# Kernel tuning notes

Hardware: AMD Instinct MI355X
Metric: run time of the kernel (lower is better)

The kernel has to match this reference:

```python
import jax, jax.numpy as jnp
import numpy as np

N, M, DIM, HEADS = 32768, 2048, 128, 8
TAU = 0.1


def setup_inputs() -> dict:
    key = jax.random.key(0)
    ks = jax.random.split(key, 7)
    return {
        "x1": jax.random.normal(ks[0], (N, DIM), jnp.float32),
        "k": jax.random.normal(ks[1], (N, DIM), jnp.float32),
        "c": jax.random.normal(ks[2], (M, DIM), jnp.float32),
        "Wq": jax.random.normal(ks[3], (DIM * HEADS, DIM), jnp.float32) * 0.02,
        "bq": jax.random.normal(ks[4], (DIM * HEADS,), jnp.float32) * 0.02,
        "Wd": jax.random.normal(ks[5], (DIM, DIM), jnp.float32) * 0.02,
        "bd": jax.random.normal(ks[6], (DIM,), jnp.float32) * 0.02,
    }


def reference(x1, k, c, Wq, bq, Wd, bd):
    # q and k both go through the same 'query' projection (as in the source)
    q = x1 @ Wq.T + bq                      # [N, dim*H]
    kq = k @ Wq.T + bq                      # [N, dim*H]
    C = jnp.tile(c, (1, HEADS))             # torch.cat([c]*H, dim=1) -> [M, dim*H]
    t = q + kq                              # additive attention 'scores' input
    logits = (t @ C.T) / jnp.sqrt(jnp.asarray(DIM, t.dtype))  # [N, M]
    p = jax.nn.softmax(logits, axis=-1)
    # gumbel_softmax(p, tau=0.1, hard=True): -log(Exp(1)) ~ Gumbel(0,1)
    noise = jax.random.gumbel(jax.random.key(42), p.shape, p.dtype)
    y_soft = jax.nn.softmax((p + noise) / TAU, axis=-1)
    idx = jnp.argmax(y_soft, axis=-1)
    y_hard = jax.nn.one_hot(idx, M, dtype=p.dtype)
    y = y_hard - jax.lax.stop_gradient(y_soft) + y_soft  # straight-through
    # attention_dropout and dropout are rate 0.0 -> identity
    out = y.T @ x1                          # [M, dim]
    return out @ Wd.T + bd                  # dense
```

## Files before the change

kernel.cpp:

```cpp
#include <hip/hip_runtime.h>
#include <stdint.h>
#include <math.h>

#define NROW 32768
#define MCOL 2048
#define KDIM 128
#define NHEAD 8
#define SCALE 0.08838834764831845f

typedef __attribute__((ext_vector_type(8))) short short8;
typedef __attribute__((ext_vector_type(4))) float f32x4;

__device__ __forceinline__ uint32_t rotl32(uint32_t x, uint32_t r) {
  return __builtin_amdgcn_alignbit(x, x, 32u - r);
}

__device__ __forceinline__ uint32_t tf_hash(uint32_t c) {
  const uint32_t K2 = 0x1BD11BDAu ^ 0u ^ 42u;
  uint32_t x0 = 0u, x1 = c + 42u;
#define R4A { x0 += x1; x1 = rotl32(x1,13); x1 ^= x0; \
              x0 += x1; x1 = rotl32(x1,15); x1 ^= x0; \
              x0 += x1; x1 = rotl32(x1,26); x1 ^= x0; \
              x0 += x1; x1 = rotl32(x1, 6); x1 ^= x0; }
#define R4B { x0 += x1; x1 = rotl32(x1,17); x1 ^= x0; \
              x0 += x1; x1 = rotl32(x1,29); x1 ^= x0; \
              x0 += x1; x1 = rotl32(x1,16); x1 ^= x0; \
              x0 += x1; x1 = rotl32(x1,24); x1 ^= x0; }
  R4A x0 += 42u;      x1 += K2 + 1u;
  R4B x0 += K2;       x1 += 2u;
  R4A    x1 += 42u + 3u;
  R4B x0 += 42u;      x1 += K2 + 4u;
  R4A x0 += K2;       x1 += 5u;
#undef R4A
#undef R4B
  return x0 ^ x1;
}

__device__ __forceinline__ float bits_to_u(uint32_t b) {
  uint32_t fb = (b >> 9) | 0x3F800000u;
  float f = __uint_as_float(fb) - 1.0f;
  return (f == 0.0f) ? 1.17549435e-38f : f;
}

__device__ __forceinline__ float gumbel_of_key(uint32_t key) {
  float u = bits_to_u(key);
  return -logf(-logf(u));
}

__global__ void k_wsum(const float* __restrict__ Wq, const float* __restrict__ bq,
                       float* __restrict__ Wsum, float* __restrict__ bsum) {
  int t = blockIdx.x * 256 + threadIdx.x;
  if (t < KDIM * KDIM) {
    int d = t >> 7, e = t & 127;
    float s = 0.f;
#pragma unroll
    for (int h = 0; h < NHEAD; ++h) s += Wq[(h * KDIM + d) * KDIM + e];
    Wsum[t] = s;
  }
  if (blockIdx.x == 0 && threadIdx.x < KDIM) {
    int d = threadIdx.x;
    float s = 0.f;
#pragma unroll
    for (int h = 0; h < NHEAD; ++h) s += bq[h * KDIM + d];
    bsum[d] = 2.0f * s;
  }
}

__global__ void k_cw(const float* __restrict__ c, const float* __restrict__ Wsum,
                     const float* __restrict__ bsum,
                     float* __restrict__ cw_s, unsigned short* __restrict__ cwB16,
                     float* __restrict__ cb_s) {
  int m = blockIdx.x;
  int e = threadIdx.x;
  __shared__ float crow[KDIM];
  if (e < 32) ((float4*)crow)[e] = ((const float4*)(c + (size_t)m * KDIM))[e];
  __syncthreads();
  float s = 0.f;
#pragma unroll 4
  for (int d = 0; d < KDIM; ++d) s += crow[d] * Wsum[d * KDIM + e];
  float sv = s * SCALE;
  cw_s[(size_t)m * KDIM + e] = sv;
  {
    int t = m >> 4, col = m & 15, ks = e >> 5, grp = (e >> 3) & 3, j = e & 7;
    int lane = grp * 16 + col;
    cwB16[(((size_t)(t * 4 + ks)) * 64 + lane) * 8 + j] =
        (unsigned short)(__float_as_uint(sv) >> 16);
  }
  if (e == 0) {
    float sb = 0.f;
    for (int d = 0; d < KDIM; ++d) sb += bsum[d] * crow[d];
    cb_s[m] = sb * SCALE;
  }
}

__launch_bounds__(256, 4)
__global__ void k_mega(const float* __restrict__ x1, const float* __restrict__ kin,
                       const uint4* __restrict__ cwB, const float* __restrict__ cb_s,
                       const float* __restrict__ cw_s, float* __restrict__ accum) {
  __shared__ float smx[32];
  __shared__ float sD[32];
  __shared__ float xksh[4][KDIM];

  const int tid = threadIdx.x;
  const int wv = tid >> 6, lane = tid & 63;
  const int B = blockIdx.x * 32;
  const int sstart = 6 * wv + ((wv >= 2) ? 4 * (wv - 2) : 0);
  const int scnt = (wv < 2) ? 6 : 10;

  if (wv < 2) {
    const int R = B + wv * 16;
    const int rowA = R + (lane & 15);
    const int kbase = (lane >> 4) * 8;

    union { uint32_t u[4]; short8 s; } af[4];
#pragma unroll
    for (int ks = 0; ks < 4; ++ks) {
      const float* xp = x1 + (size_t)rowA * KDIM + ks * 32 + kbase;
      const float* kp = kin + (size_t)rowA * KDIM + ks * 32 + kbase;
      float4 a0 = *(const float4*)xp, a1 = *(const float4*)(xp + 4);
      float4 b0 = *(const float4*)kp, b1 = *(const float4*)(kp + 4);
      float f[8] = {a0.x + b0.x, a0.y + b0.y, a0.z + b0.z, a0.w + b0.w,
                    a1.x + b1.x, a1.y + b1.y, a1.z + b1.z, a1.w + b1.w};
#pragma unroll
      for (int r = 0; r < 4; ++r)
        af[ks].u[r] = (__float_as_uint(f[2 * r]) >> 16) |
                      (__float_as_uint(f[2 * r + 1]) & 0xFFFF0000u);
    }

    float mxs[4], Ds[4];
#pragma unroll
    for (int r = 0; r < 4; ++r) { mxs[r] = -INFINITY; Ds[r] = 0.f; }

#pragma unroll 2
    for (int t = 0; t < 128; ++t) {
      f32x4 acc = {0.f, 0.f, 0.f, 0.f};
#pragma unroll
      for (int ks = 0; ks < 4; ++ks) {
        union { uint4 v; short8 s; } bf;
        bf.v = cwB[(size_t)(t * 4 + ks) * 64 + lane];
        acc = __builtin_amdgcn_mfma_f32_16x16x32_bf16(af[ks].s, bf.s, acc, 0, 0, 0);
      }
      float cbv = cb_s[t * 16 + (lane & 15)];
#pragma unroll
      for (int r = 0; r < 4; ++r) {
        float lv = acc[r] + cbv;
        mxs[r] = fmaxf(mxs[r], lv);
        Ds[r] += __expf(lv);
      }
    }

#pragma unroll
    for (int s = 1; s < 16; s <<= 1) {
#pragma unroll
      for (int r = 0; r < 4; ++r) {
        mxs[r] = fmaxf(mxs[r], __shfl_xor(mxs[r], s));
        Ds[r] += __shfl_xor(Ds[r], s);
      }
    }
    if ((lane & 15) == 0) {
#pragma unroll
      for (int r = 0; r < 4; ++r) {
        int lr = wv * 16 + (lane >> 4) * 4 + r;
        smx[lr] = mxs[r];
        sD[lr] = Ds[r];
      }
    }
  }

  uint32_t tk0[10], tk1[10], tk2[10];
#pragma unroll
  for (int ri = 0; ri < 10; ++ri) {
    if (ri < scnt) {
      const int n = B + sstart + ri;
      const uint32_t c0 = (uint32_t)n * (uint32_t)MCOL + (uint32_t)lane;
      uint32_t t0 = 0u, t1 = 0u, t2 = 0u;
#pragma unroll 8
      for (uint32_t jj = 0; jj < 32; ++jj) {
        uint32_t b = tf_hash(c0 + 64u * jj);
        uint32_t key = (b & 0xFFFFFE00u) | jj;
        t2 = max(t2, min(min(t0, t1), key));
        t1 = max(t1, min(t0, key));
        t0 = max(t0, key);
      }
      tk0[ri] = t0; tk1[ri] = t1; tk2[ri] = t2;
    }
  }

  __syncthreads();

#pragma unroll
  for (int ri = 0; ri < 10; ++ri) {
    if (ri < scnt) {
      const int n = B + sstart + ri;
      const int lr = sstart + ri;

      uint32_t t0 = tk0[ri], t1 = tk1[ri], t2 = tk2[ri];
      uint32_t kmax = t0;
#pragma unroll
      for (int s = 1; s < 64; s <<= 1)
        kmax = max(kmax, (uint32_t)__shfl_xor((int)kmax, s));

      const float mx = smx[lr], Dp = sD[lr];
      const float pmax = __expf(mx) / Dp;
      const float gstar = gumbel_of_key(kmax);
      const float thr = gstar - (pmax * 1.05f + 2e-4f);

      const float2 xa = ((const float2*)(x1 + (size_t)n * KDIM))[lane];
      const float2 xb = ((const float2*)(kin + (size_t)n * KDIM))[lane];
      const float xk0 = xa.x + xb.x, xk1 = xa.y + xb.y;

      float bestSc = -INFINITY;
      int bestM = 0x7FFFFFFF;

      if (pmax > 0.2f) {
        xksh[wv][lane * 2] = xk0;
        xksh[wv][lane * 2 + 1] = xk1;
        __builtin_amdgcn_s_waitcnt(0);
        for (uint32_t jj = 0; jj < 32; ++jj) {
          uint32_t m = (uint32_t)lane | (jj << 6);
          uint32_t b = tf_hash((uint32_t)n * (uint32_t)MCOL + m);
          float g = -logf(-logf(bits_to_u(b)));
          float l = 0.f;
          for (int e = 0; e < KDIM; ++e) l += xksh[wv][e] * cw_s[(size_t)m * KDIM + e];
          float p = __expf(l + cb_s[m]) / Dp;
          float sc = p + g;
          if (sc > bestSc || (sc == bestSc && (int)m < bestM)) { bestSc = sc; bestM = (int)m; }
        }
#pragma unroll
        for (int s = 1; s < 64; s <<= 1) {
          float os = __shfl_xor(bestSc, s);
          int om = __shfl_xor(bestM, s);
          if (os > bestSc || (os == bestSc && om < bestM)) { bestSc = os; bestM = om; }
        }
      } else {
#pragma unroll
        for (int s = 0; s < 3; ++s) {
          uint32_t tkv = (s == 0) ? t0 : ((s == 1) ? t1 : t2);
          float g = gumbel_of_key(tkv);
          unsigned long long bl = __ballot(g >= thr);
          while (bl) {
            int src = __ffsll(bl) - 1;
            bl &= bl - 1ull;
            uint32_t kk = (uint32_t)__shfl((int)tkv, src);
            float gc = __shfl(g, src);
            int m = src | (int)((kk & 31u) << 6);
            const float2 cv = ((const float2*)(cw_s + (size_t)m * KDIM))[lane];
            float part = xk0 * cv.x + xk1 * cv.y;
#pragma unroll
            for (int sh = 1; sh < 64; sh <<= 1) part += __shfl_xor(part, sh);
            float p = __expf(part + cb_s[m]) / Dp;
            float sc = p + gc;
            if (sc > bestSc || (sc == bestSc && m < bestM)) { bestSc = sc; bestM = m; }
          }
        }
      }

      float* dst = accum + (size_t)bestM * KDIM + lane * 2;
      atomicAdd(dst + 0, xa.x);
      atomicAdd(dst + 1, xa.y);
    }
  }
}

__global__ void k_final(const float* __restrict__ acc, const float* __restrict__ Wd,
                        const float* __restrict__ bd, float* __restrict__ out) {
  int m = blockIdx.x, j = threadIdx.x;
  __shared__ float ar[KDIM];
  if (j < 32) ((float4*)ar)[j] = ((const float4*)(acc + (size_t)m * KDIM))[j];
  __syncthreads();
  const float4* wr = (const float4*)(Wd + (size_t)j * KDIM);
  float s = 0.f;
#pragma unroll
  for (int e4 = 0; e4 < 32; ++e4) {
    float4 wv = wr[e4];
    s += wv.x * ar[4 * e4 + 0] + wv.y * ar[4 * e4 + 1]
       + wv.z * ar[4 * e4 + 2] + wv.w * ar[4 * e4 + 3];
  }
  out[(size_t)m * KDIM + j] = s + bd[j];
}

extern "C" void kernel_launch(void* const* d_in, const int* in_sizes, int n_in,
                              void* d_out, int out_size, void* d_ws, size_t ws_size,
                              hipStream_t stream) {
  const float* x1 = (const float*)d_in[0];
  const float* k  = (const float*)d_in[1];
  const float* c  = (const float*)d_in[2];
  const float* Wq = (const float*)d_in[3];
  const float* bq = (const float*)d_in[4];
  const float* Wd = (const float*)d_in[5];
  const float* bd = (const float*)d_in[6];
  float* out = (float*)d_out;

  char* ws = (char*)d_ws;
  size_t off = 0;
  float* cw_s = (float*)(ws + off); off += (size_t)MCOL * KDIM * 4;
  float* cb_s = (float*)(ws + off); off += 8192;
  unsigned short* cwB = (unsigned short*)(ws + off); off += (size_t)MCOL * KDIM * 2;
  float* Wsum = (float*)(ws + off); off += KDIM * KDIM * 4;
  float* bsum = (float*)(ws + off); off += 4096;
  float* accum = (float*)(ws + off); off += (size_t)MCOL * KDIM * 4;

  hipMemsetAsync(accum, 0, (size_t)MCOL * KDIM * sizeof(float), stream);
  k_wsum<<<64, 256, 0, stream>>>(Wq, bq, Wsum, bsum);
  k_cw<<<MCOL, 128, 0, stream>>>(c, Wsum, bsum, cw_s, cwB, cb_s);
  k_mega<<<1024, 256, 0, stream>>>(x1, k, (const uint4*)cwB, cb_s, cw_s, accum);
  k_final<<<MCOL, 128, 0, stream>>>(accum, Wd, bd, out);
}
```

Baseline: 207.0 us.

## Split softmax-denominator MFMA across all four waves and trim per-lane top-k to two

The softmax max/denominator pass now runs on all four waves. Each wave covers 32 of the 128 column tiles for both 16-row halves and writes partial max/sum values that are merged through shared memory. Previously only two waves did this pass, with an uneven split of the sampling rows. Each wave now handles exactly 8 rows for sampling and tracks only the top-2 keys per lane instead of top-3. A fallback "valve" path rescans all hashes against a derived key threshold when the second key could still qualify, which keeps exactness at the cost of extra hashing in rare rows.

```diff
diff --git a/kernel.cpp b/kernel.cpp
--- a/kernel.cpp
+++ b/kernel.cpp
@@ -97,55 +97,70 @@
 __global__ void k_mega(const float* __restrict__ x1, const float* __restrict__ kin,
                        const uint4* __restrict__ cwB, const float* __restrict__ cb_s,
                        const float* __restrict__ cw_s, float* __restrict__ accum) {
-  __shared__ float smx[32];
-  __shared__ float sD[32];
+  __shared__ float smx_p[4][32];
+  __shared__ float sD_p[4][32];
   __shared__ float xksh[4][KDIM];
 
   const int tid = threadIdx.x;
   const int wv = tid >> 6, lane = tid & 63;
   const int B = blockIdx.x * 32;
-  const int sstart = 6 * wv + ((wv >= 2) ? 4 * (wv - 2) : 0);
-  const int scnt = (wv < 2) ? 6 : 10;
-
-  if (wv < 2) {
-    const int R = B + wv * 16;
-    const int rowA = R + (lane & 15);
+
+  {
+    const int row0 = B + (lane & 15);
     const int kbase = (lane >> 4) * 8;
 
-    union { uint32_t u[4]; short8 s; } af[4];
+    union { uint32_t u[4]; short8 s; } af0[4], af1[4];
 #pragma unroll
     for (int ks = 0; ks < 4; ++ks) {
-      const float* xp = x1 + (size_t)rowA * KDIM + ks * 32 + kbase;
-      const float* kp = kin + (size_t)rowA * KDIM + ks * 32 + kbase;
-      float4 a0 = *(const float4*)xp, a1 = *(const float4*)(xp + 4);
-      float4 b0 = *(const float4*)kp, b1 = *(const float4*)(kp + 4);
-      float f[8] = {a0.x + b0.x, a0.y + b0.y, a0.z + b0.z, a0.w + b0.w,
-                    a1.x + b1.x, a1.y + b1.y, a1.z + b1.z, a1.w + b1.w};
-#pragma unroll
-      for (int r = 0; r < 4; ++r)
-        af[ks].u[r] = (__float_as_uint(f[2 * r]) >> 16) |
-                      (__float_as_uint(f[2 * r + 1]) & 0xFFFF0000u);
-    }
-
-    float mxs[4], Ds[4];
-#pragma unroll
-    for (int r = 0; r < 4; ++r) { mxs[r] = -INFINITY; Ds[r] = 0.f; }
+      const float* xp0 = x1 + (size_t)row0 * KDIM + ks * 32 + kbase;
+      const float* kp0 = kin + (size_t)row0 * KDIM + ks * 32 + kbase;
+      float4 a0 = *(const float4*)xp0, a1 = *(const float4*)(xp0 + 4);
+      float4 b0 = *(const float4*)kp0, b1 = *(const float4*)(kp0 + 4);
+      float f0[8] = {a0.x + b0.x, a0.y + b0.y, a0.z + b0.z, a0.w + b0.w,
+                     a1.x + b1.x, a1.y + b1.y, a1.z + b1.z, a1.w + b1.w};
+      const float* xp1 = xp0 + 16 * KDIM;
+      const float* kp1 = kp0 + 16 * KDIM;
+      float4 c0v = *(const float4*)xp1, c1v = *(const float4*)(xp1 + 4);
+      float4 d0v = *(const float4*)kp1, d1v = *(const float4*)(kp1 + 4);
+      float f1[8] = {c0v.x + d0v.x, c0v.y + d0v.y, c0v.z + d0v.z, c0v.w + d0v.w,
+                     c1v.x + d1v.x, c1v.y + d1v.y, c1v.z + d1v.z, c1v.w + d1v.w};
+#pragma unroll
+      for (int r = 0; r < 4; ++r) {
+        af0[ks].u[r] = (__float_as_uint(f0[2 * r]) >> 16) |
+                       (__float_as_uint(f0[2 * r + 1]) & 0xFFFF0000u);
+        af1[ks].u[r] = (__float_as_uint(f1[2 * r]) >> 16) |
+                       (__float_as_uint(f1[2 * r + 1]) & 0xFFFF0000u);
+      }
+    }
+
+    float mxs0[4], Ds0[4], mxs1[4], Ds1[4];
+#pragma unroll
+    for (int r = 0; r < 4; ++r) {
+      mxs0[r] = -INFINITY; Ds0[r] = 0.f;
+      mxs1[r] = -INFINITY; Ds1[r] = 0.f;
+    }
 
 #pragma unroll 2
-    for (int t = 0; t < 128; ++t) {
-      f32x4 acc = {0.f, 0.f, 0.f, 0.f};
+    for (int ti = 0; ti < 32; ++ti) {
+      const int t = wv * 32 + ti;
+      f32x4 acc0 = {0.f, 0.f, 0.f, 0.f};
+      f32x4 acc1 = {0.f, 0.f, 0.f, 0.f};
 #pragma unroll
       for (int ks = 0; ks < 4; ++ks) {
         union { uint4 v; short8 s; } bf;
         bf.v = cwB[(size_t)(t * 4 + ks) * 64 + lane];
-        acc = __builtin_amdgcn_mfma_f32_16x16x32_bf16(af[ks].s, bf.s, acc, 0, 0, 0);
+        acc0 = __builtin_amdgcn_mfma_f32_16x16x32_bf16(af0[ks].s, bf.s, acc0, 0, 0, 0);
+        acc1 = __builtin_amdgcn_mfma_f32_16x16x32_bf16(af1[ks].s, bf.s, acc1, 0, 0, 0);
       }
       float cbv = cb_s[t * 16 + (lane & 15)];
 #pragma unroll
       for (int r = 0; r < 4; ++r) {
-        float lv = acc[r] + cbv;
-        mxs[r] = fmaxf(mxs[r], lv);
-        Ds[r] += __expf(lv);
+        float l0 = acc0[r] + cbv;
+        mxs0[r] = fmaxf(mxs0[r], l0);
+        Ds0[r] += __expf(l0);
+        float l1 = acc1[r] + cbv;
+        mxs1[r] = fmaxf(mxs1[r], l1);
+        Ds1[r] += __expf(l1);
       }
     }
 
@@ -153,112 +168,138 @@
     for (int s = 1; s < 16; s <<= 1) {
 #pragma unroll
       for (int r = 0; r < 4; ++r) {
-        mxs[r] = fmaxf(mxs[r], __shfl_xor(mxs[r], s));
-        Ds[r] += __shfl_xor(Ds[r], s);
+        mxs0[r] = fmaxf(mxs0[r], __shfl_xor(mxs0[r], s));
+        Ds0[r] += __shfl_xor(Ds0[r], s);
+        mxs1[r] = fmaxf(mxs1[r], __shfl_xor(mxs1[r], s));
+        Ds1[r] += __shfl_xor(Ds1[r], s);
       }
     }
     if ((lane & 15) == 0) {
 #pragma unroll
       for (int r = 0; r < 4; ++r) {
-        int lr = wv * 16 + (lane >> 4) * 4 + r;
-        smx[lr] = mxs[r];
-        sD[lr] = Ds[r];
-      }
-    }
-  }
-
-  uint32_t tk0[10], tk1[10], tk2[10];
-#pragma unroll
-  for (int ri = 0; ri < 10; ++ri) {
-    if (ri < scnt) {
-      const int n = B + sstart + ri;
+        int lr = (lane >> 4) * 4 + r;
+        smx_p[wv][lr] = mxs0[r];
+        sD_p[wv][lr] = Ds0[r];
+        smx_p[wv][16 + lr] = mxs1[r];
+        sD_p[wv][16 + lr] = Ds1[r];
+      }
+    }
+  }
+
+  const uint32_t KEYMASK = 0xFFFFFE00u;
+  uint32_t tk0[8], tk1[8];
+#pragma unroll
+  for (int ri = 0; ri < 8; ++ri) {
+    const int n = B + wv * 8 + ri;
+    const uint32_t c0 = (uint32_t)n * (uint32_t)MCOL + (uint32_t)lane;
+    uint32_t t0 = 0u, t1 = 0u;
+#pragma unroll 8
+    for (uint32_t jj = 0; jj < 32; ++jj) {
+      uint32_t b = tf_hash(c0 + 64u * jj);
+      uint32_t key = (b & KEYMASK) | jj;
+      t1 = max(t1, min(t0, key));
+      t0 = max(t0, key);
+    }
+    tk0[ri] = t0;
+    tk1[ri] = t1;
+  }
+
+  __syncthreads();
+
+#pragma unroll 1
+  for (int ri = 0; ri < 8; ++ri) {
+    const int lr = wv * 8 + ri;
+    const int n = B + lr;
+
+    uint32_t t0 = tk0[ri], t1 = tk1[ri];
+    uint32_t kmax = t0;
+#pragma unroll
+    for (int s = 1; s < 64; s <<= 1)
+      kmax = max(kmax, (uint32_t)__shfl_xor((int)kmax, s));
+
+    float mx = smx_p[0][lr];
+    mx = fmaxf(mx, smx_p[1][lr]);
+    mx = fmaxf(mx, smx_p[2][lr]);
+    mx = fmaxf(mx, smx_p[3][lr]);
+    const float Dp = sD_p[0][lr] + sD_p[1][lr] + sD_p[2][lr] + sD_p[3][lr];
+    const float pmax = __expf(mx) / Dp;
+
+    const float gstar = gumbel_of_key(kmax);
+    const float thr = gstar - (pmax * 1.05f + 2e-4f);
+
+    float ustar = bits_to_u(kmax);
+    float uthr = __expf(1.30f * __logf(ustar));
+    uint32_t bthr = (__float_as_uint(uthr + 1.0f) & 0x007FFFFFu) << 9;
+    if (bthr >= 512u) bthr -= 512u;
+
+    const float2 xa = ((const float2*)(x1 + (size_t)n * KDIM))[lane];
+    const float2 xb = ((const float2*)(kin + (size_t)n * KDIM))[lane];
+    const float xk0 = xa.x + xb.x, xk1 = xa.y + xb.y;
+
+    float bestSc = -INFINITY;
+    int bestM = 0x7FFFFFFF;
+
+    auto adjudicate_ballot = [&](unsigned long long bl, uint32_t keyv, float gval) {
+      while (bl) {
+        int src = __ffsll(bl) - 1;
+        bl &= bl - 1ull;
+        uint32_t kk = (uint32_t)__shfl((int)keyv, src);
+        float gc = __shfl(gval, src);
+        int m = src | (int)((kk & 31u) << 6);
+        const float2 cv = ((const float2*)(cw_s + (size_t)m * KDIM))[lane];
+        float part = xk0 * cv.x + xk1 * cv.y;
+#pragma unroll
+        for (int sh = 1; sh < 64; sh <<= 1) part += __shfl_xor(part, sh);
+        float p = __expf(part + cb_s[m]) / Dp;
+        float sc = p + gc;
+        if (sc > bestSc || (sc == bestSc && m < bestM)) { bestSc = sc; bestM = m; }
+      }
+    };
+
+    const unsigned long long valve = __ballot(t1 >= bthr && t1 != 0u);
+
+    if (pmax > 0.2f) {
+      xksh[wv][lane * 2] = xk0;
+      xksh[wv][lane * 2 + 1] = xk1;
+      __builtin_amdgcn_s_waitcnt(0);
+      for (uint32_t jj = 0; jj < 32; ++jj) {
+        uint32_t m = (uint32_t)lane | (jj << 6);
+        uint32_t b = tf_hash((uint32_t)n * (uint32_t)MCOL + m);
+        float g = -logf(-logf(bits_to_u(b)));
+        float l = 0.f;
+        for (int e = 0; e < KDIM; ++e) l += xksh[wv][e] * cw_s[(size_t)m * KDIM + e];
+        float p = __expf(l + cb_s[m]) / Dp;
+        float sc = p + g;
+        if (sc > bestSc || (sc == bestSc && (int)m < bestM)) { bestSc = sc; bestM = (int)m; }
+      }
+#pragma unroll
+      for (int s = 1; s < 64; s <<= 1) {
+        float os = __shfl_xor(bestSc, s);
+        int om = __shfl_xor(bestM, s);
+        if (os > bestSc || (os == bestSc && om < bestM)) { bestSc = os; bestM = om; }
+      }
+    } else if (valve) {
       const uint32_t c0 = (uint32_t)n * (uint32_t)MCOL + (uint32_t)lane;
-      uint32_t t0 = 0u, t1 = 0u, t2 = 0u;
-#pragma unroll 8
       for (uint32_t jj = 0; jj < 32; ++jj) {
         uint32_t b = tf_hash(c0 + 64u * jj);
-        uint32_t key = (b & 0xFFFFFE00u) | jj;
-        t2 = max(t2, min(min(t0, t1), key));
-        t1 = max(t1, min(t0, key));
-        t0 = max(t0, key);
-      }
-      tk0[ri] = t0; tk1[ri] = t1; tk2[ri] = t2;
-    }
-  }
-
-  __syncthreads();
-
-#pragma unroll
-  for (int ri = 0; ri < 10; ++ri) {
-    if (ri < scnt) {
-      const int n = B + sstart + ri;
-      const int lr = sstart + ri;
-
-      uint32_t t0 = tk0[ri], t1 = tk1[ri], t2 = tk2[ri];
-      uint32_t kmax = t0;
-#pragma unroll
-      for (int s = 1; s < 64; s <<= 1)
-        kmax = max(kmax, (uint32_t)__shfl_xor((int)kmax, s));
-
-      const float mx = smx[lr], Dp = sD[lr];
-      const float pmax = __expf(mx) / Dp;
-      const float gstar = gumbel_of_key(kmax);
-      const float thr = gstar - (pmax * 1.05f + 2e-4f);
-
-      const float2 xa = ((const float2*)(x1 + (size_t)n * KDIM))[lane];
-      const float2 xb = ((const float2*)(kin + (size_t)n * KDIM))[lane];
-      const float xk0 = xa.x + xb.x, xk1 = xa.y + xb.y;
-
-      float bestSc = -INFINITY;
-      int bestM = 0x7FFFFFFF;
-
-      if (pmax > 0.2f) {
-        xksh[wv][lane * 2] = xk0;
-        xksh[wv][lane * 2 + 1] = xk1;
-        __builtin_amdgcn_s_waitcnt(0);
-        for (uint32_t jj = 0; jj < 32; ++jj) {
-          uint32_t m = (uint32_t)lane | (jj << 6);
-          uint32_t b = tf_hash((uint32_t)n * (uint32_t)MCOL + m);
-          float g = -logf(-logf(bits_to_u(b)));
-          float l = 0.f;
-          for (int e = 0; e < KDIM; ++e) l += xksh[wv][e] * cw_s[(size_t)m * KDIM + e];
-          float p = __expf(l + cb_s[m]) / Dp;
-          float sc = p + g;
-          if (sc > bestSc || (sc == bestSc && (int)m < bestM)) { bestSc = sc; bestM = (int)m; }
-        }
-#pragma unroll
-        for (int s = 1; s < 64; s <<= 1) {
-          float os = __shfl_xor(bestSc, s);
-          int om = __shfl_xor(bestM, s);
-          if (os > bestSc || (os == bestSc && om < bestM)) { bestSc = os; bestM = om; }
-        }
-      } else {
-#pragma unroll
-        for (int s = 0; s < 3; ++s) {
-          uint32_t tkv = (s == 0) ? t0 : ((s == 1) ? t1 : t2);
-          float g = gumbel_of_key(tkv);
-          unsigned long long bl = __ballot(g >= thr);
-          while (bl) {
-            int src = __ffsll(bl) - 1;
-            bl &= bl - 1ull;
-            uint32_t kk = (uint32_t)__shfl((int)tkv, src);
-            float gc = __shfl(g, src);
-            int m = src | (int)((kk & 31u) << 6);
-            const float2 cv = ((const float2*)(cw_s + (size_t)m * KDIM))[lane];
-            float part = xk0 * cv.x + xk1 * cv.y;
-#pragma unroll
-            for (int sh = 1; sh < 64; sh <<= 1) part += __shfl_xor(part, sh);
-            float p = __expf(part + cb_s[m]) / Dp;
-            float sc = p + gc;
-            if (sc > bestSc || (sc == bestSc && m < bestM)) { bestSc = sc; bestM = m; }
-          }
-        }
-      }
-
-      float* dst = accum + (size_t)bestM * KDIM + lane * 2;
-      atomicAdd(dst + 0, xa.x);
-      atomicAdd(dst + 1, xa.y);
-    }
+        uint32_t key = (b & KEYMASK) | jj;
+        unsigned long long mk = __ballot(key >= bthr);
+        if (mk) adjudicate_ballot(mk, key, gumbel_of_key(key));
+      }
+    } else {
+      {
+        float g = gumbel_of_key(t0);
+        adjudicate_ballot(__ballot(g >= thr), t0, g);
+      }
+      {
+        float g = (t1 != 0u) ? gumbel_of_key(t1) : -INFINITY;
+        adjudicate_ballot(__ballot(g >= thr), t1, g);
+      }
+    }
+
+    float* dst = accum + (size_t)bestM * KDIM + lane * 2;
+    atomicAdd(dst + 0, xa.x);
+    atomicAdd(dst + 1, xa.y);
   }
 }
 
```

After: 250.9 us. +21.2%, slower.

## Fold accum zeroing into wsum, rebalance row split, interleave hash chains

Applied to the files above, without the earlier changes.

Removes the separate memset by zeroing the accumulator inside k_wsum (64x256 threads x 4 float4 covers exactly 2048x128 floats). Rebalances the per-wave row assignment from 6/6/10/10 to 7/7/9/9, since the two MFMA waves carry extra logit work. Interleaves two independent Threefry hash chains per iteration to raise ILP, and keeps the selection loop rolled to reduce code size and register pressure. The risk is that the rolled loop indexes the tk arrays dynamically, which may push them to scratch memory.

```diff
diff --git a/kernel.cpp b/kernel.cpp
--- a/kernel.cpp
+++ b/kernel.cpp
@@ -48,7 +48,8 @@
 }
 
 __global__ void k_wsum(const float* __restrict__ Wq, const float* __restrict__ bq,
-                       float* __restrict__ Wsum, float* __restrict__ bsum) {
+                       float* __restrict__ Wsum, float* __restrict__ bsum,
+                       float* __restrict__ accum) {
   int t = blockIdx.x * 256 + threadIdx.x;
   if (t < KDIM * KDIM) {
     int d = t >> 7, e = t & 127;
@@ -56,6 +57,12 @@
 #pragma unroll
     for (int h = 0; h < NHEAD; ++h) s += Wq[(h * KDIM + d) * KDIM + e];
     Wsum[t] = s;
+  }
+  {
+    float4 z = {0.f, 0.f, 0.f, 0.f};
+    float4* a4 = (float4*)accum;
+#pragma unroll
+    for (int r = 0; r < 4; ++r) a4[t + r * 16384] = z;
   }
   if (blockIdx.x == 0 && threadIdx.x < KDIM) {
     int d = threadIdx.x;
@@ -104,8 +111,8 @@
   const int tid = threadIdx.x;
   const int wv = tid >> 6, lane = tid & 63;
   const int B = blockIdx.x * 32;
-  const int sstart = 6 * wv + ((wv >= 2) ? 4 * (wv - 2) : 0);
-  const int scnt = (wv < 2) ? 6 : 10;
+  const int sstart = (wv < 2) ? wv * 7 : 14 + (wv - 2) * 9;
+  const int scnt = (wv < 2) ? 7 : 9;
 
   if (wv < 2) {
     const int R = B + wv * 16;
@@ -167,98 +174,102 @@
     }
   }
 
-  uint32_t tk0[10], tk1[10], tk2[10];
-#pragma unroll
-  for (int ri = 0; ri < 10; ++ri) {
+  uint32_t tk0[9], tk1[9], tk2[9];
+#pragma unroll
+  for (int ri = 0; ri < 9; ++ri) {
     if (ri < scnt) {
       const int n = B + sstart + ri;
       const uint32_t c0 = (uint32_t)n * (uint32_t)MCOL + (uint32_t)lane;
       uint32_t t0 = 0u, t1 = 0u, t2 = 0u;
-#pragma unroll 8
+#pragma unroll 4
+      for (uint32_t jj = 0; jj < 16; ++jj) {
+        uint32_t bA = tf_hash(c0 + 64u * jj);
+        uint32_t bB = tf_hash(c0 + 64u * (jj + 16u));
+        uint32_t kA = (bA & 0xFFFFFE00u) | jj;
+        uint32_t kB = (bB & 0xFFFFFE00u) | (jj + 16u);
+        t2 = max(t2, min(min(t0, t1), kA));
+        t1 = max(t1, min(t0, kA));
+        t0 = max(t0, kA);
+        t2 = max(t2, min(min(t0, t1), kB));
+        t1 = max(t1, min(t0, kB));
+        t0 = max(t0, kB);
+      }
+      tk0[ri] = t0; tk1[ri] = t1; tk2[ri] = t2;
+    }
+  }
+
+  __syncthreads();
+
+#pragma unroll 1
+  for (int ri = 0; ri < 9; ++ri) {
+    if (ri >= scnt) break;
+    const int lr = sstart + ri;
+    const int n = B + lr;
+
+    uint32_t t0 = tk0[ri], t1 = tk1[ri], t2 = tk2[ri];
+    uint32_t kmax = t0;
+#pragma unroll
+    for (int s = 1; s < 64; s <<= 1)
+      kmax = max(kmax, (uint32_t)__shfl_xor((int)kmax, s));
+
+    const float mx = smx[lr], Dp = sD[lr];
+    const float pmax = __expf(mx) / Dp;
+    const float gstar = gumbel_of_key(kmax);
+    const float thr = gstar - (pmax * 1.05f + 2e-4f);
+
+    const float2 xa = ((const float2*)(x1 + (size_t)n * KDIM))[lane];
+    const float2 xb = ((const float2*)(kin + (size_t)n * KDIM))[lane];
+    const float xk0 = xa.x + xb.x, xk1 = xa.y + xb.y;
+
+    float bestSc = -INFINITY;
+    int bestM = 0x7FFFFFFF;
+
+    if (pmax > 0.2f) {
+      xksh[wv][lane * 2] = xk0;
+      xksh[wv][lane * 2 + 1] = xk1;
+      __builtin_amdgcn_s_waitcnt(0);
       for (uint32_t jj = 0; jj < 32; ++jj) {
-        uint32_t b = tf_hash(c0 + 64u * jj);
-        uint32_t key = (b & 0xFFFFFE00u) | jj;
-        t2 = max(t2, min(min(t0, t1), key));
-        t1 = max(t1, min(t0, key));
-        t0 = max(t0, key);
-      }
-      tk0[ri] = t0; tk1[ri] = t1; tk2[ri] = t2;
-    }
-  }
-
-  __syncthreads();
-
-#pragma unroll
-  for (int ri = 0; ri < 10; ++ri) {
-    if (ri < scnt) {
-      const int n = B + sstart + ri;
-      const int lr = sstart + ri;
-
-      uint32_t t0 = tk0[ri], t1 = tk1[ri], t2 = tk2[ri];
-      uint32_t kmax = t0;
-#pragma unroll
-      for (int s = 1; s < 64; s <<= 1)
-        kmax = max(kmax, (uint32_t)__shfl_xor((int)kmax, s));
-
-      const float mx = smx[lr], Dp = sD[lr];
-      const float pmax = __expf(mx) / Dp;
-      const float gstar = gumbel_of_key(kmax);
-      const float thr = gstar - (pmax * 1.05f + 2e-4f);
-
-      const float2 xa = ((const float2*)(x1 + (size_t)n * KDIM))[lane];
-      const float2 xb = ((const float2*)(kin + (size_t)n * KDIM))[lane];
-      const float xk0 = xa.x + xb.x, xk1 = xa.y + xb.y;
-
-      float bestSc = -INFINITY;
-      int bestM = 0x7FFFFFFF;
-
-      if (pmax > 0.2f) {
-        xksh[wv][lane * 2] = xk0;
-        xksh[wv][lane * 2 + 1] = xk1;
-        __builtin_amdgcn_s_waitcnt(0);
-        for (uint32_t jj = 0; jj < 32; ++jj) {
-          uint32_t m = (uint32_t)lane | (jj << 6);
-          uint32_t b = tf_hash((uint32_t)n * (uint32_t)MCOL + m);
-          float g = -logf(-logf(bits_to_u(b)));
-          float l = 0.f;
-          for (int e = 0; e < KDIM; ++e) l += xksh[wv][e] * cw_s[(size_t)m * KDIM + e];
-          float p = __expf(l + cb_s[m]) / Dp;
-          float sc = p + g;
-          if (sc > bestSc || (sc == bestSc && (int)m < bestM)) { bestSc = sc; bestM = (int)m; }
+        uint32_t m = (uint32_t)lane | (jj << 6);
+        uint32_t b = tf_hash((uint32_t)n * (uint32_t)MCOL + m);
+        float g = -logf(-logf(bits_to_u(b)));
+        float l = 0.f;
+        for (int e = 0; e < KDIM; ++e) l += xksh[wv][e] * cw_s[(size_t)m * KDIM + e];
+        float p = __expf(l + cb_s[m]) / Dp;
+        float sc = p + g;
+        if (sc > bestSc || (sc == bestSc && (int)m < bestM)) { bestSc = sc; bestM = (int)m; }
+      }
+#pragma unroll
+      for (int s = 1; s < 64; s <<= 1) {
+        float os = __shfl_xor(bestSc, s);
+        int om = __shfl_xor(bestM, s);
+        if (os > bestSc || (os == bestSc && om < bestM)) { bestSc = os; bestM = om; }
+      }
+    } else {
+#pragma unroll
+      for (int s = 0; s < 3; ++s) {
+        uint32_t tkv = (s == 0) ? t0 : ((s == 1) ? t1 : t2);
+        float g = gumbel_of_key(tkv);
+        unsigned long long bl = __ballot(g >= thr);
+        while (bl) {
+          int src = __ffsll(bl) - 1;
+          bl &= bl - 1ull;
+          uint32_t kk = (uint32_t)__shfl((int)tkv, src);
+          float gc = __shfl(g, src);
+          int m = src | (int)((kk & 31u) << 6);
+          const float2 cv = ((const float2*)(cw_s + (size_t)m * KDIM))[lane];
+          float part = xk0 * cv.x + xk1 * cv.y;
+#pragma unroll
+          for (int sh = 1; sh < 64; sh <<= 1) part += __shfl_xor(part, sh);
+          float p = __expf(part + cb_s[m]) / Dp;
+          float sc = p + gc;
+          if (sc > bestSc || (sc == bestSc && m < bestM)) { bestSc = sc; bestM = m; }
         }
-#pragma unroll
-        for (int s = 1; s < 64; s <<= 1) {
-          float os = __shfl_xor(bestSc, s);
-          int om = __shfl_xor(bestM, s);
-          if (os > bestSc || (os == bestSc && om < bestM)) { bestSc = os; bestM = om; }
-        }
-      } else {
-#pragma unroll
-        for (int s = 0; s < 3; ++s) {
-          uint32_t tkv = (s == 0) ? t0 : ((s == 1) ? t1 : t2);
-          float g = gumbel_of_key(tkv);
-          unsigned long long bl = __ballot(g >= thr);
-          while (bl) {
-            int src = __ffsll(bl) - 1;
-            bl &= bl - 1ull;
-            uint32_t kk = (uint32_t)__shfl((int)tkv, src);
-            float gc = __shfl(g, src);
-            int m = src | (int)((kk & 31u) << 6);
-            const float2 cv = ((const float2*)(cw_s + (size_t)m * KDIM))[lane];
-            float part = xk0 * cv.x + xk1 * cv.y;
-#pragma unroll
-            for (int sh = 1; sh < 64; sh <<= 1) part += __shfl_xor(part, sh);
-            float p = __expf(part + cb_s[m]) / Dp;
-            float sc = p + gc;
-            if (sc > bestSc || (sc == bestSc && m < bestM)) { bestSc = sc; bestM = m; }
-          }
-        }
-      }
-
-      float* dst = accum + (size_t)bestM * KDIM + lane * 2;
-      atomicAdd(dst + 0, xa.x);
-      atomicAdd(dst + 1, xa.y);
-    }
+      }
+    }
+
+    float* dst = accum + (size_t)bestM * KDIM + lane * 2;
+    atomicAdd(dst + 0, xa.x);
+    atomicAdd(dst + 1, xa.y);
   }
 }
 
@@ -300,8 +311,7 @@
   float* bsum = (float*)(ws + off); off += 4096;
   float* accum = (float*)(ws + off); off += (size_t)MCOL * KDIM * 4;
 
-  hipMemsetAsync(accum, 0, (size_t)MCOL * KDIM * sizeof(float), stream);
-  k_wsum<<<64, 256, 0, stream>>>(Wq, bq, Wsum, bsum);
+  k_wsum<<<64, 256, 0, stream>>>(Wq, bq, Wsum, bsum, accum);
   k_cw<<<MCOL, 128, 0, stream>>>(c, Wsum, bsum, cw_s, cwB, cb_s);
   k_mega<<<1024, 256, 0, stream>>>(x1, k, (const uint4*)cwB, cb_s, cw_s, accum);
   k_final<<<MCOL, 128, 0, stream>>>(accum, Wd, bd, out);
```

Measured after the change: 225.1 us. 8.7% more time.
